# Performance work log

Hardware: AMD Instinct MI355X
Metric: run time of the kernel (lower is better)

## Reference

```python
import jax, jax.numpy as jnp
import numpy as np

EPS = 1e-6
K_HOPS = 2  # SGConv K


def setup_inputs() -> dict:
    key = jax.random.key(0)
    k1, k2, k3, k4 = jax.random.split(key, 4)
    B, Kk, C, T = 32, 8, 64, 250
    E, H = 4096, 128
    x = jax.random.normal(k1, (B, Kk, C, T), dtype=jnp.float32)
    edge_index = jax.random.randint(k2, (2, E), 0, C, dtype=jnp.int64)
    edge_weights = jax.random.uniform(k3, (E,), dtype=jnp.float32)
    W = jax.random.normal(k4, (H, Kk * T), dtype=jnp.float32) * 0.02
    b = jnp.zeros((H,), dtype=jnp.float32)
    return {"x": x, "edge_index": edge_index, "edge_weights": edge_weights, "W": W, "b": b}


def reference(x, edge_index, edge_weights, W, b):
    B, Kk, C, T = x.shape
    N = C  # nodes
    x = x.reshape(B, N, Kk * T)  # (B, N, F)

    # clamp non-positive edge weights to epsilon (mirrors in-place .data clamp)
    w = jnp.where(edge_weights <= 0, EPS, edge_weights)

    # gcn_norm with self loops (fill value 1.0)
    src, dst = edge_index[0], edge_index[1]
    loop = jnp.arange(N, dtype=edge_index.dtype)
    src = jnp.concatenate([src, loop])
    dst = jnp.concatenate([dst, loop])
    w = jnp.concatenate([w, jnp.ones((N,), w.dtype)])
    deg = jnp.zeros((N,), w.dtype).at[dst].add(w)
    dinv = jnp.where(deg > 0, deg ** -0.5, jnp.zeros_like(deg))
    norm = dinv[src] * w * dinv[dst]  # (E+N,)

    # K hops of gather -> weight -> scatter-add aggregation
    for _ in range(K_HOPS):
        msg = x[:, src, :] * norm[None, :, None]        # (B, E+N, F)
        x = jnp.zeros_like(x).at[:, dst, :].add(msg)    # (B, N, F)

    # final linear: y = x @ W^T + b
    return jnp.einsum('bnf,hf->bnh', x, W) + b
```

## Files before the change

kernel.cpp:

```cpp
#include <hip/hip_runtime.h>
#include <hip/hip_bf16.h>

#define EPSW 1e-6f

typedef __attribute__((ext_vector_type(4))) float floatx4;
typedef __attribute__((ext_vector_type(8))) short shortx8;

__device__ __forceinline__ unsigned short f2bf(float f) {
    unsigned int u = __float_as_uint(f);
    u = (u + 0x7fffu + ((u >> 16) & 1u)) >> 16;
    return (unsigned short)u;
}

__device__ __forceinline__ void gl_lds16(const void* g, void* l) {
    __builtin_amdgcn_global_load_lds(
        (const __attribute__((address_space(1))) unsigned int*)g,
        (__attribute__((address_space(3))) unsigned int*)l, 16, 0, 0);
}

__global__ __launch_bounds__(512) void prep(const float* __restrict__ x,
                                            const float* __restrict__ W,
                                            const int* __restrict__ ei,
                                            const float* __restrict__ ew,
                                            unsigned short* __restrict__ xt,
                                            unsigned short* __restrict__ wt,
                                            float* __restrict__ Mt) {
    __shared__ __align__(16) unsigned char smem[64 * 264 * 2];
    const int bid = blockIdx.x;
    const int t   = threadIdx.x;

    if (bid < 256) {
        unsigned short(*tile)[264] = (unsigned short(*)[264])smem;
        const int rb   = (bid >> 3) * 64;
        const int kgb  = (bid & 7) * 32;
        const int kbas = kgb * 8;
#pragma unroll
        for (int i = 0; i < 8; ++i) {
            const int idx = i * 512 + t;
            const int r   = idx >> 6;
            const int kc  = (idx & 63) * 4;
            const int k   = kbas + kc;
            floatx4 v = (floatx4){0.f, 0.f, 0.f, 0.f};
            if (k < 2000)
                v = *(const floatx4*)(x + (size_t)(rb + r) * 2000 + k);
            tile[r][kc + 0] = f2bf(v.x);
            tile[r][kc + 1] = f2bf(v.y);
            tile[r][kc + 2] = f2bf(v.z);
            tile[r][kc + 3] = f2bf(v.w);
        }
        __syncthreads();
#pragma unroll
        for (int i = 0; i < 4; ++i) {
            const int kg_l = i * 8 + (t >> 6);
            const int r    = t & 63;
            const shortx8 g = *(const shortx8*)&tile[r][kg_l * 8];
            *(shortx8*)(xt + ((size_t)(kgb + kg_l) * 2048 + rb + r) * 8) = g;
        }
    } else if (bid < 272) {
#pragma unroll
        for (int i = 0; i < 4; ++i) {
            const int G  = (bid - 256) * 2048 + i * 512 + t;
            const int kg = G >> 7;
            const int h  = G & 127;
            const int k  = kg * 8;
            floatx4 v0 = (floatx4){0.f, 0.f, 0.f, 0.f};
            floatx4 v1 = (floatx4){0.f, 0.f, 0.f, 0.f};
            if (k < 2000) {
                v0 = *(const floatx4*)(W + (size_t)h * 2000 + k);
                v1 = *(const floatx4*)(W + (size_t)h * 2000 + k + 4);
            }
            unsigned short* p = wt + ((size_t)kg * 128 + h) * 8;
            p[0] = f2bf(v0.x); p[1] = f2bf(v0.y); p[2] = f2bf(v0.z); p[3] = f2bf(v0.w);
            p[4] = f2bf(v1.x); p[5] = f2bf(v1.y); p[6] = f2bf(v1.z); p[7] = f2bf(v1.w);
        }
    } else {
        float* A    = (float*)smem;
        float* deg  = (float*)(smem + 16384);
        float* dinv = deg + 64;
        if (t < 64) deg[t] = 1.0f;
        for (int i = t; i < 4096; i += 512) A[i] = 0.0f;
        __syncthreads();
        const int* srcp = ei;
        const int* dstp = ei + 4096;
#pragma unroll
        for (int i = 0; i < 8; ++i) {
            const int e = i * 512 + t;
            float w = ew[e];
            w = (w <= 0.0f) ? EPSW : w;
            atomicAdd(&deg[dstp[e]], w);
        }
        __syncthreads();
        if (t < 64) dinv[t] = 1.0f / sqrtf(deg[t]);
        __syncthreads();
#pragma unroll
        for (int i = 0; i < 8; ++i) {
            const int e = i * 512 + t;
            float w = ew[e];
            w = (w <= 0.0f) ? EPSW : w;
            const int s = srcp[e], d = dstp[e];
            atomicAdd(&A[d * 64 + s], dinv[s] * w * dinv[d]);
        }
        if (t < 64) atomicAdd(&A[t * 64 + t], dinv[t] * dinv[t]);
        __syncthreads();
#pragma unroll
        for (int i = 0; i < 8; ++i) {
            const int idx = i * 512 + t;
            const int n = idx >> 6, c = idx & 63;
            float s = 0.0f;
#pragma unroll 8
            for (int k = 0; k < 64; ++k) s += A[n * 64 + k] * A[k * 64 + c];
            Mt[c * 64 + n] = s;
        }
    }
}

__global__ __launch_bounds__(256) void gemm_lds(
        const unsigned short* __restrict__ xt,
        const unsigned short* __restrict__ wt,
        float* __restrict__ zp) {
    __shared__ __align__(16) unsigned char smem[2][24576];
    const int t    = threadIdx.x;
    const int wave = t >> 6, lane = t & 63;
    const int m = lane & 15, q = lane >> 4;
    const int bid   = blockIdx.x;
    const int ks    = bid >> 5;
    const int rbase = (bid & 31) * 64;
    const int kg0   = ks * 32;

    floatx4 acc[4][2];
#pragma unroll
    for (int rt = 0; rt < 4; ++rt)
#pragma unroll
        for (int hh = 0; hh < 2; ++hh)
            acc[rt][hh] = (floatx4){0.f, 0.f, 0.f, 0.f};

#define ISSUE_CHUNK(c)                                                        \
    {                                                                         \
        unsigned char* sb = smem[(c) & 1];                                    \
        const int ckg = kg0 + (c) * 8;                                        \
        for (int j = wave; j < 24; j += 4) {                                  \
            if (j < 8) {                                                      \
                gl_lds16(xt + ((size_t)(ckg + j) * 2048 + rbase + lane) * 8,  \
                         sb + j * 1024);                                      \
            } else {                                                          \
                const int kgl = (j - 8) >> 1, hf = (j - 8) & 1;               \
                gl_lds16(wt + ((size_t)(ckg + kgl) * 128 + hf * 64 + lane) * 8,\
                         sb + 8192 + kgl * 2048 + hf * 1024);                 \
            }                                                                 \
        }                                                                     \
    }

    ISSUE_CHUNK(0);
    for (int c = 0; c < 4; ++c) {
        __builtin_amdgcn_s_waitcnt(0);
        __syncthreads();
        if (c < 3) ISSUE_CHUNK(c + 1);
        const unsigned char* sb = smem[c & 1];
#pragma unroll
        for (int p = 0; p < 2; ++p) {
            shortx8 a[4];
#pragma unroll
            for (int rt = 0; rt < 4; ++rt)
                a[rt] = *(const shortx8*)(sb + (p * 4 + q) * 1024 + (rt * 16 + m) * 16);
            shortx8 bb[2];
#pragma unroll
            for (int hh = 0; hh < 2; ++hh)
                bb[hh] = *(const shortx8*)(sb + 8192 + (p * 4 + q) * 2048 +
                                           ((wave + hh * 4) * 16 + m) * 16);
#pragma unroll
            for (int rt = 0; rt < 4; ++rt)
#pragma unroll
                for (int hh = 0; hh < 2; ++hh)
                    acc[rt][hh] = __builtin_amdgcn_mfma_f32_16x16x32_bf16(
                        a[rt], bb[hh], acc[rt][hh], 0, 0, 0);
        }
        __syncthreads();
    }

#pragma unroll
    for (int rt = 0; rt < 4; ++rt)
#pragma unroll
        for (int hh = 0; hh < 2; ++hh) {
            const int h = (wave + hh * 4) * 16 + m;
#pragma unroll
            for (int v = 0; v < 4; ++v) {
                const int row = rbase + rt * 16 + q * 4 + v;
                zp[((size_t)ks * 2048 + row) * 128 + h] = acc[rt][hh][v];
            }
        }
}

__global__ __launch_bounds__(256) void apply_M(const float* __restrict__ zp,
                                               const float* __restrict__ Mtg,
                                               const float* __restrict__ bias,
                                               float* __restrict__ y) {
    __shared__ float Ms[4096];
    __shared__ float zs[64][16];
    const int b  = blockIdx.x;
    const int hc = blockIdx.y;
    const int t  = threadIdx.x;
#pragma unroll
    for (int i = 0; i < 16; ++i) Ms[i * 256 + t] = Mtg[i * 256 + t];
#pragma unroll
    for (int i = 0; i < 4; ++i) {
        const int idx = i * 256 + t;
        const int mr = idx >> 4, hh = idx & 15;
        float s = 0.0f;
#pragma unroll
        for (int ks = 0; ks < 8; ++ks)
            s += zp[((size_t)ks * 2048 + b * 64 + mr) * 128 + hc * 16 + hh];
        zs[mr][hh] = s;
    }
    __syncthreads();
    const int h  = t & 15;
    const int n0 = (t >> 4) * 4;
    const float bv = bias[hc * 16 + h];
    float s0 = bv, s1 = bv, s2 = bv, s3 = bv;
#pragma unroll
    for (int mm = 0; mm < 64; ++mm) {
        const float zv = zs[mm][h];
        s0 += Ms[mm * 64 + n0 + 0] * zv;
        s1 += Ms[mm * 64 + n0 + 1] * zv;
        s2 += Ms[mm * 64 + n0 + 2] * zv;
        s3 += Ms[mm * 64 + n0 + 3] * zv;
    }
    float* yp = y + (size_t)b * 8192 + (size_t)n0 * 128 + hc * 16 + h;
    yp[0]   = s0;
    yp[128] = s1;
    yp[256] = s2;
    yp[384] = s3;
}

extern "C" void kernel_launch(void* const* d_in, const int* in_sizes, int n_in,
                              void* d_out, int out_size, void* d_ws, size_t ws_size,
                              hipStream_t stream) {
    const float* x    = (const float*)d_in[0];
    const int*   ei   = (const int*)d_in[1];
    const float* ew   = (const float*)d_in[2];
    const float* W    = (const float*)d_in[3];
    const float* bias = (const float*)d_in[4];
    float* y = (float*)d_out;

    float* zp = (float*)d_ws;
    float* Mt = zp + 2097152;
    unsigned short* xt = (unsigned short*)(Mt + 4096);
    unsigned short* wt = xt + 4194304;

    prep<<<273, 512, 0, stream>>>(x, W, ei, ew, xt, wt, Mt);
    gemm_lds<<<256, 256, 0, stream>>>(xt, wt, zp);
    apply_M<<<dim3(32, 8), 256, 0, stream>>>(zp, Mt, bias, y);
}
```

Before: 97.69 us.

## Fuse x bf16 conversion into GEMM loads and split M computation across blocks

The GEMM kernel now reads fp32 x straight from global memory into registers, converts it to bf16 and writes it to LDS. This removes the separate prep pass that transposed and converted x into a bf16 workspace, along with that workspace's write and re-read. The prep kernel shrinks to W conversion plus four blocks that each compute 16 rows of the A^2 matrix, so the 64x64 product is no longer done by a single block. The trade-off is that x loads in the GEMM are now register-staged rather than async direct-to-LDS, and each of the four graph blocks redundantly rebuilds the adjacency matrix.

```diff
diff --git a/kernel.cpp b/kernel.cpp
--- a/kernel.cpp
+++ b/kernel.cpp
@@ -4,6 +4,7 @@
 #define EPSW 1e-6f
 
 typedef __attribute__((ext_vector_type(4))) float floatx4;
+typedef __attribute__((ext_vector_type(4))) unsigned int uintx4;
 typedef __attribute__((ext_vector_type(8))) short shortx8;
 
 __device__ __forceinline__ unsigned short f2bf(float f) {
@@ -12,54 +13,29 @@
     return (unsigned short)u;
 }
 
+__device__ __forceinline__ unsigned int pk2(float lo, float hi) {
+    return (unsigned int)f2bf(lo) | ((unsigned int)f2bf(hi) << 16);
+}
+
 __device__ __forceinline__ void gl_lds16(const void* g, void* l) {
     __builtin_amdgcn_global_load_lds(
         (const __attribute__((address_space(1))) unsigned int*)g,
         (__attribute__((address_space(3))) unsigned int*)l, 16, 0, 0);
 }
 
-__global__ __launch_bounds__(512) void prep(const float* __restrict__ x,
-                                            const float* __restrict__ W,
+__global__ __launch_bounds__(512) void prep(const float* __restrict__ W,
                                             const int* __restrict__ ei,
                                             const float* __restrict__ ew,
-                                            unsigned short* __restrict__ xt,
                                             unsigned short* __restrict__ wt,
                                             float* __restrict__ Mt) {
-    __shared__ __align__(16) unsigned char smem[64 * 264 * 2];
+    __shared__ float sA[4096 + 128];
     const int bid = blockIdx.x;
     const int t   = threadIdx.x;
 
-    if (bid < 256) {
-        unsigned short(*tile)[264] = (unsigned short(*)[264])smem;
-        const int rb   = (bid >> 3) * 64;
-        const int kgb  = (bid & 7) * 32;
-        const int kbas = kgb * 8;
-#pragma unroll
-        for (int i = 0; i < 8; ++i) {
-            const int idx = i * 512 + t;
-            const int r   = idx >> 6;
-            const int kc  = (idx & 63) * 4;
-            const int k   = kbas + kc;
-            floatx4 v = (floatx4){0.f, 0.f, 0.f, 0.f};
-            if (k < 2000)
-                v = *(const floatx4*)(x + (size_t)(rb + r) * 2000 + k);
-            tile[r][kc + 0] = f2bf(v.x);
-            tile[r][kc + 1] = f2bf(v.y);
-            tile[r][kc + 2] = f2bf(v.z);
-            tile[r][kc + 3] = f2bf(v.w);
-        }
-        __syncthreads();
+    if (bid < 16) {
 #pragma unroll
         for (int i = 0; i < 4; ++i) {
-            const int kg_l = i * 8 + (t >> 6);
-            const int r    = t & 63;
-            const shortx8 g = *(const shortx8*)&tile[r][kg_l * 8];
-            *(shortx8*)(xt + ((size_t)(kgb + kg_l) * 2048 + rb + r) * 8) = g;
-        }
-    } else if (bid < 272) {
-#pragma unroll
-        for (int i = 0; i < 4; ++i) {
-            const int G  = (bid - 256) * 2048 + i * 512 + t;
+            const int G  = bid * 2048 + i * 512 + t;
             const int kg = G >> 7;
             const int h  = G & 127;
             const int k  = kg * 8;
@@ -74,8 +50,9 @@
             p[4] = f2bf(v1.x); p[5] = f2bf(v1.y); p[6] = f2bf(v1.z); p[7] = f2bf(v1.w);
         }
     } else {
-        float* A    = (float*)smem;
-        float* deg  = (float*)(smem + 16384);
+        const int bb = bid - 16;
+        float* A    = sA;
+        float* deg  = sA + 4096;
         float* dinv = deg + 64;
         if (t < 64) deg[t] = 1.0f;
         for (int i = t; i < 4096; i += 512) A[i] = 0.0f;
@@ -102,20 +79,23 @@
         }
         if (t < 64) atomicAdd(&A[t * 64 + t], dinv[t] * dinv[t]);
         __syncthreads();
-#pragma unroll
-        for (int i = 0; i < 8; ++i) {
-            const int idx = i * 512 + t;
-            const int n = idx >> 6, c = idx & 63;
-            float s = 0.0f;
+        const int c  = t & 63;
+        const int n0 = bb * 16 + (t >> 6);
+        const int n1 = n0 + 8;
+        float s0 = 0.0f, s1 = 0.0f;
 #pragma unroll 8
-            for (int k = 0; k < 64; ++k) s += A[n * 64 + k] * A[k * 64 + c];
-            Mt[c * 64 + n] = s;
-        }
+        for (int k = 0; k < 64; ++k) {
+            const float akc = A[k * 64 + c];
+            s0 += A[n0 * 64 + k] * akc;
+            s1 += A[n1 * 64 + k] * akc;
+        }
+        Mt[c * 64 + n0] = s0;
+        Mt[c * 64 + n1] = s1;
     }
 }
 
 __global__ __launch_bounds__(256) void gemm_lds(
-        const unsigned short* __restrict__ xt,
+        const float* __restrict__ x,
         const unsigned short* __restrict__ wt,
         float* __restrict__ zp) {
     __shared__ __align__(16) unsigned char smem[2][24576];
@@ -127,6 +107,9 @@
     const int rbase = (bid & 31) * 64;
     const int kg0   = ks * 32;
 
+    const int kgl = lane >> 3;
+    const int rr0 = wave * 8 + (lane & 7);
+
     floatx4 acc[4][2];
 #pragma unroll
     for (int rt = 0; rt < 4; ++rt)
@@ -134,27 +117,55 @@
         for (int hh = 0; hh < 2; ++hh)
             acc[rt][hh] = (floatx4){0.f, 0.f, 0.f, 0.f};
 
-#define ISSUE_CHUNK(c)                                                        \
+    floatx4 va0, va1, vb0, vb1;
+
+#define LOAD_A(c)                                                             \
     {                                                                         \
-        unsigned char* sb = smem[(c) & 1];                                    \
-        const int ckg = kg0 + (c) * 8;                                        \
-        for (int j = wave; j < 24; j += 4) {                                  \
-            if (j < 8) {                                                      \
-                gl_lds16(xt + ((size_t)(ckg + j) * 2048 + rbase + lane) * 8,  \
-                         sb + j * 1024);                                      \
-            } else {                                                          \
-                const int kgl = (j - 8) >> 1, hf = (j - 8) & 1;               \
-                gl_lds16(wt + ((size_t)(ckg + kgl) * 128 + hf * 64 + lane) * 8,\
-                         sb + 8192 + kgl * 2048 + hf * 1024);                 \
-            }                                                                 \
+        const int k_ = ks * 256 + (c) * 64 + kgl * 8;                         \
+        const float* px_ = x + (size_t)(rbase + rr0) * 2000 + k_;             \
+        if (k_ < 2000) {                                                      \
+            va0 = *(const floatx4*)px_;                                       \
+            va1 = *(const floatx4*)(px_ + 4);                                 \
+            vb0 = *(const floatx4*)(px_ + 64000);                             \
+            vb1 = *(const floatx4*)(px_ + 64004);                             \
+        } else {                                                              \
+            va0 = va1 = vb0 = vb1 = (floatx4){0.f, 0.f, 0.f, 0.f};            \
         }                                                                     \
     }
 
-    ISSUE_CHUNK(0);
+#define WRITE_A(c)                                                            \
+    {                                                                         \
+        unsigned char* sb_ = smem[(c) & 1];                                   \
+        uintx4 g0_, g1_;                                                      \
+        g0_.x = pk2(va0.x, va0.y); g0_.y = pk2(va0.z, va0.w);                 \
+        g0_.z = pk2(va1.x, va1.y); g0_.w = pk2(va1.z, va1.w);                 \
+        g1_.x = pk2(vb0.x, vb0.y); g1_.y = pk2(vb0.z, vb0.w);                 \
+        g1_.z = pk2(vb1.x, vb1.y); g1_.w = pk2(vb1.z, vb1.w);                 \
+        *(uintx4*)(sb_ + kgl * 1024 + rr0 * 16) = g0_;                        \
+        *(uintx4*)(sb_ + kgl * 1024 + (rr0 + 32) * 16) = g1_;                 \
+    }
+
+#define ISSUE_B(c)                                                            \
+    {                                                                         \
+        unsigned char* sb_ = smem[(c) & 1];                                   \
+        const int ckg_ = kg0 + (c) * 8;                                       \
+        for (int j = wave; j < 16; j += 4) {                                  \
+            const int kb_ = j >> 1, hf_ = j & 1;                              \
+            gl_lds16(wt + ((size_t)(ckg_ + kb_) * 128 + hf_ * 64 + lane) * 8, \
+                     sb_ + 8192 + kb_ * 2048 + hf_ * 1024);                   \
+        }                                                                     \
+    }
+
+    LOAD_A(0);
+    ISSUE_B(0);
     for (int c = 0; c < 4; ++c) {
         __builtin_amdgcn_s_waitcnt(0);
-        __syncthreads();
-        if (c < 3) ISSUE_CHUNK(c + 1);
+        WRITE_A(c);
+        if (c < 3) {
+            LOAD_A(c + 1);
+            ISSUE_B(c + 1);
+        }
+        __syncthreads();
         const unsigned char* sb = smem[c & 1];
 #pragma unroll
         for (int p = 0; p < 2; ++p) {
@@ -176,6 +187,9 @@
         }
         __syncthreads();
     }
+#undef LOAD_A
+#undef WRITE_A
+#undef ISSUE_B
 
 #pragma unroll
     for (int rt = 0; rt < 4; ++rt)
@@ -243,10 +257,9 @@
 
     float* zp = (float*)d_ws;
     float* Mt = zp + 2097152;
-    unsigned short* xt = (unsigned short*)(Mt + 4096);
-    unsigned short* wt = xt + 4194304;
-
-    prep<<<273, 512, 0, stream>>>(x, W, ei, ew, xt, wt, Mt);
-    gemm_lds<<<256, 256, 0, stream>>>(xt, wt, zp);
+    unsigned short* wt = (unsigned short*)(Mt + 4096);
+
+    prep<<<20, 512, 0, stream>>>(W, ei, ew, wt, Mt);
+    gemm_lds<<<256, 256, 0, stream>>>(x, wt, zp);
     apply_M<<<dim3(32, 8), 256, 0, stream>>>(zp, Mt, bias, y);
 }
```

New measurement: 93.45 us. 1.05x faster.
